# Performance work log

Measured on AMD Instinct MI355X. Metric: run time of the kernel, lower is better.

## Reference

```python
import jax, jax.numpy as jnp
import numpy as np

H, DH, RK, RD = 16, 128, 512, 64  # num_heads, head_dim, kv_lora_rank, rope_dim


def apply_rope(x, cos, sin):
    # x: [..., L, ..., rope_dim]; cos/sin: [L, rope_dim//2]
    cos = cos[None, :, None, :]
    sin = sin[None, :, None, :]
    x1, x2 = x[..., 0::2], x[..., 1::2]
    out_real = x1 * cos - x2 * sin
    out_imag = x1 * sin + x2 * cos
    return jnp.stack([out_real, out_imag], axis=-1).reshape(x.shape)


def setup_inputs() -> dict:
    key = jax.random.key(0)
    ks = jax.random.split(key, 7)
    B, L, E, MAXLEN = 2, 2048, 2048, 4096
    x = jax.random.normal(ks[0], (B, L, E), dtype=jnp.float32)
    cos_table = jax.random.uniform(ks[1], (MAXLEN, RD // 2), dtype=jnp.float32)
    sin_table = jax.random.uniform(ks[2], (MAXLEN, RD // 2), dtype=jnp.float32)
    wq = jax.random.normal(ks[3], (E, H * (DH + RD)), dtype=jnp.float32) / np.sqrt(E)
    wkv_down = jax.random.normal(ks[4], (E, RK + RD), dtype=jnp.float32) / np.sqrt(E)
    w_up = jax.random.normal(ks[5], (RK, H * (2 * DH + RD)), dtype=jnp.float32) / np.sqrt(RK)
    w_out = jax.random.normal(ks[6], (H * (DH + RD), E), dtype=jnp.float32) / np.sqrt(H * (DH + RD))
    return {"x": x, "cos_table": cos_table, "sin_table": sin_table,
            "wq": wq, "wkv_down": wkv_down, "w_up": w_up, "w_out": w_out}


def reference(x, cos_table, sin_table, wq, wkv_down, w_up, w_out):
    # Prefill path (use_cache=False): idx = 0, kv comes from current tokens only.
    B, L, E = x.shape
    cos = cos_table[:L]
    sin = sin_table[:L]

    # Queries: per-head content part + rope part
    q_all = (x @ wq).reshape(B, L, H, DH + RD)
    q_head, q_rope = q_all[..., :DH], q_all[..., DH:]
    q_rope = apply_rope(q_rope, cos, sin)
    q = jnp.concatenate([q_head, q_rope], axis=-1)  # [B,L,H,DH+RD]

    # Compressed KV latent + shared rope key
    kv_lat = x @ wkv_down                            # [B,L,RK+RD]
    c_kv = kv_lat[..., :RK]
    k_rope = kv_lat[..., RK:]
    k_rope = apply_rope(k_rope[:, :, None, :], cos, sin)[:, :, 0, :]  # [B,L,RD]

    # Up-project latent to per-head K/V
    up = (c_kv @ w_up).reshape(B, L, H, 2 * DH + RD)
    k_head = up[..., :DH]
    v_head = up[..., DH:2 * DH]
    v_rope = up[..., 2 * DH:]
    k_rope_b = jnp.broadcast_to(k_rope[:, :, None, :], (B, L, H, RD))
    k = jnp.concatenate([k_head, k_rope_b], axis=-1)  # [B,L,H,DH+RD]
    v = jnp.concatenate([v_head, v_rope], axis=-1)    # [B,L,H,DH+RD]

    # Causal attention (query_indices = arange(L), key_indices = arange(L))
    scale = 1.0 / jnp.sqrt(jnp.float32(DH + RD))
    scores = jnp.einsum('blhd,bshd->bhls', q, k) * scale
    idxs = jnp.arange(L)
    bias = jnp.where(idxs[:, None] >= idxs[None, :], 0.0, -1000000000.0)
    attn = jax.nn.softmax(scores + bias[None, None, :, :], axis=-1)
    out = jnp.einsum('bhls,bshd->blhd', attn, v)  # [B,L,H,DH+RD]
    return out.reshape(B, L, -1) @ w_out
```

## Files before the change

### kernel.cpp

```cpp
#include <hip/hip_runtime.h>
#include <stdint.h>

#define H_ 16
#define DH_ 128
#define RK_ 512
#define RD_ 64
#define B_ 2
#define L_ 2048
#define E_ 2048
#define DQ_ 192
#define NQ_ (H_*DQ_)
#define NKV_ 576
#define NKVP_ 640
#define QKVP_ 3840
#define NUP_ (H_*(2*DH_+RD_))
#define M_ (B_*L_)

typedef unsigned short u16;
typedef __bf16 bf16x8 __attribute__((ext_vector_type(8)));
typedef float floatx4 __attribute__((ext_vector_type(4)));

__device__ __forceinline__ u16 f2bf(float f) {
    union { float f; uint32_t u; } v; v.f = f;
    uint32_t u = v.u;
    u = (u + 0x7fffu + ((u >> 16) & 1u)) >> 16;
    return (u16)u;
}
__device__ __forceinline__ float bf2f(u16 b) {
    union { uint32_t u; float f; } v; v.u = ((uint32_t)b) << 16; return v.f;
}

__device__ __forceinline__ void gld_lds16(const void* g, void* l) {
    __builtin_amdgcn_global_load_lds((__attribute__((address_space(1))) void*)(g),
                                     (__attribute__((address_space(3))) void*)(l),
                                     16, 0, 0);
}

__global__ void convert_bf16(const float* __restrict__ in, u16* __restrict__ out, int n4) {
    int i = blockIdx.x * blockDim.x + threadIdx.x;
    if (i >= n4) return;
    float4 v = ((const float4*)in)[i];
    uint2 o;
    o.x = (uint32_t)f2bf(v.x) | ((uint32_t)f2bf(v.y) << 16);
    o.y = (uint32_t)f2bf(v.z) | ((uint32_t)f2bf(v.w) << 16);
    ((uint2*)out)[i] = o;
}

__global__ void transpose_w(const float* __restrict__ W, u16* __restrict__ Wt,
                            int K, int N, int Npad) {
    __shared__ float tile[32][33];
    int n0 = blockIdx.x * 32, k0 = blockIdx.y * 32;
    int tx = threadIdx.x, ty = threadIdx.y;
    for (int i = 0; i < 4; i++) {
        int k = k0 + ty + i * 8, n = n0 + tx;
        tile[ty + i * 8][tx] = (n < N) ? W[(size_t)k * N + n] : 0.f;
    }
    __syncthreads();
    for (int i = 0; i < 4; i++) {
        int n = n0 + ty + i * 8, k = k0 + tx;
        Wt[(size_t)n * K + k] = f2bf(tile[tx][ty + i * 8]);
    }
}

__global__ __launch_bounds__(256) void gemm_bt(const u16* __restrict__ A,
                                               const u16* __restrict__ Bt,
                                               float* __restrict__ C,
                                               int M, int N, int K) {
    __shared__ __align__(16) u16 As[128 * 32];
    __shared__ __align__(16) u16 Bs[128 * 32];
    const int tid = threadIdx.x;
    const int wave = tid >> 6, lane = tid & 63;
    const int quad = lane >> 4, l16 = lane & 15;
    const int m0 = blockIdx.y * 128, n0 = blockIdx.x * 128;
    const int wm = (wave >> 1) * 64, wn = (wave & 1) * 64;

    floatx4 zero4 = {0.f, 0.f, 0.f, 0.f};
    floatx4 acc[4][4];
    for (int i = 0; i < 4; i++) for (int j = 0; j < 4; j++) acc[i][j] = zero4;

    const u16* Ab = A + (size_t)m0 * K;
    const u16* Bb = Bt + (size_t)n0 * K;

    for (int k0 = 0; k0 < K; k0 += 32) {
        for (int it = 0; it < 2; ++it) {
            int c = it * 256 + tid;
            int row = c >> 2, cr = c & 3;
            gld_lds16(Ab + (size_t)row * K + k0 + cr * 8, As + c * 8);
            gld_lds16(Bb + (size_t)row * K + k0 + cr * 8, Bs + c * 8);
        }
        __syncthreads();
        bf16x8 af[4], bfr[4];
        for (int i = 0; i < 4; i++) af[i]  = *(const bf16x8*)(As + (wm + i * 16 + l16) * 32 + quad * 8);
        for (int j = 0; j < 4; j++) bfr[j] = *(const bf16x8*)(Bs + (wn + j * 16 + l16) * 32 + quad * 8);
        for (int i = 0; i < 4; i++)
            for (int j = 0; j < 4; j++)
                acc[i][j] = __builtin_amdgcn_mfma_f32_16x16x32_bf16(af[i], bfr[j], acc[i][j], 0, 0, 0);
        __syncthreads();
    }
    for (int i = 0; i < 4; i++)
        for (int j = 0; j < 4; j++) {
            int mrow = m0 + wm + i * 16 + quad * 4;
            int ncol = n0 + wn + j * 16 + l16;
            float* Cp = C + (size_t)mrow * N + ncol;
            for (int r = 0; r < 4; r++) Cp[(size_t)r * N] = acc[i][j][r];
        }
}

__global__ __launch_bounds__(512, 4) void gemm256(const u16* __restrict__ A,
                                                  const u16* __restrict__ Bt,
                                                  float* __restrict__ C,
                                                  int M, int N, int K) {
    __shared__ __align__(16) u16 As[3][256 * 32];
    __shared__ __align__(16) u16 Bs[3][128 * 32];
    const int tid = threadIdx.x;
    const int wave = tid >> 6, lane = tid & 63;
    const int quad = lane >> 4, l16 = lane & 15;
    const int wm = (wave >> 1) * 64, wn = (wave & 1) * 64;

    int nwg = gridDim.x * gridDim.y;
    int flat = blockIdx.y * gridDim.x + blockIdx.x;
    int q = nwg >> 3, r = nwg & 7;
    int xcd = flat & 7, pos = flat >> 3;
    int wg = (xcd < r) ? xcd * (q + 1) + pos : r * (q + 1) + (xcd - r) * q + pos;
    const int m0 = (wg & 15) * 256;
    const int n0 = (wg >> 4) * 128;

    const u16* Ab = A + (size_t)m0 * K;
    const u16* Bb = Bt + (size_t)n0 * K;

    const int qsw = (quad ^ ((l16 >> 1) & 3)) * 8;

    floatx4 zero4 = {0.f, 0.f, 0.f, 0.f};
    floatx4 acc[4][4];
#pragma unroll
    for (int i = 0; i < 4; i++)
#pragma unroll
        for (int j = 0; j < 4; j++) acc[i][j] = zero4;

    auto stage = [&](int t, int b) {
        const u16* Ak = Ab + t * 32;
        const u16* Bk = Bb + t * 32;
#pragma unroll
        for (int it = 0; it < 2; ++it) {
            int c = it * 512 + tid;
            int row = c >> 2, blk = c & 3;
            int bg = blk ^ ((row >> 1) & 3);
            gld_lds16(Ak + (size_t)row * K + bg * 8, As[b] + row * 32 + blk * 8);
        }
        {
            int row = tid >> 2, blk = tid & 3;
            int bg = blk ^ ((row >> 1) & 3);
            gld_lds16(Bk + (size_t)row * K + bg * 8, Bs[b] + row * 32 + blk * 8);
        }
    };

    const int NT = K >> 5;
    stage(0, 0);
    stage(1, 1);
    int rb = 0;
    for (int t = 0; t < NT; ++t) {
        if (t + 2 < NT) {
            stage(t + 2, rb ? rb - 1 : 2);
            asm volatile("s_waitcnt vmcnt(6)" ::: "memory");
        } else if (t + 1 < NT) {
            asm volatile("s_waitcnt vmcnt(3)" ::: "memory");
        } else {
            asm volatile("s_waitcnt vmcnt(0)" ::: "memory");
        }
        __builtin_amdgcn_s_barrier();

        const u16* Ar = As[rb];
        const u16* Br = Bs[rb];
        bf16x8 af[4], bfv[4];
#pragma unroll
        for (int i = 0; i < 4; i++) af[i]  = *(const bf16x8*)(Ar + (wm + i * 16 + l16) * 32 + qsw);
#pragma unroll
        for (int j = 0; j < 4; j++) bfv[j] = *(const bf16x8*)(Br + (wn + j * 16 + l16) * 32 + qsw);
        __builtin_amdgcn_s_setprio(1);
#pragma unroll
        for (int i = 0; i < 4; i++)
#pragma unroll
            for (int j = 0; j < 4; j++)
                acc[i][j] = __builtin_amdgcn_mfma_f32_16x16x32_bf16(af[i], bfv[j], acc[i][j], 0, 0, 0);
        __builtin_amdgcn_s_setprio(0);
        __builtin_amdgcn_s_barrier();
        rb = (rb == 2) ? 0 : rb + 1;
    }

#pragma unroll
    for (int i = 0; i < 4; i++)
#pragma unroll
        for (int j = 0; j < 4; j++) {
            int mrow = m0 + wm + i * 16 + quad * 4;
            int ncol = n0 + wn + j * 16 + l16;
            float* Cp = C + (size_t)mrow * N + ncol;
            for (int rr = 0; rr < 4; rr++) Cp[(size_t)rr * N] = acc[i][j][rr];
        }
}

__global__ void build_q(const float* __restrict__ qkv, const float* __restrict__ cosT,
                        const float* __restrict__ sinT, u16* __restrict__ qb) {
    const float QS = 0.07216878364870323f * 1.4426950408889634f;
    int idx = blockIdx.x * blockDim.x + threadIdx.x;
    if (idx >= M_ * H_ * 96) return;
    int p = idx % 96; int t = idx / 96; int h = t % H_; int row = t / H_;
    int l = row & (L_ - 1); int b = row >> 11;
    const float* src = qkv + (size_t)row * QKVP_ + h * DQ_;
    u16* dst = qb + ((size_t)(b * H_ + h) * L_ + l) * DQ_;
    int d = 2 * p;
    float x1 = src[d], x2 = src[d + 1];
    if (d < DH_) { dst[d] = f2bf(x1 * QS); dst[d + 1] = f2bf(x2 * QS); }
    else {
        int i = (d - DH_) >> 1;
        float c = cosT[(size_t)l * 32 + i], s = sinT[(size_t)l * 32 + i];
        dst[d]     = f2bf((x1 * c - x2 * s) * QS);
        dst[d + 1] = f2bf((x1 * s + x2 * c) * QS);
    }
}

__global__ void build_ckv(const float* __restrict__ qkv, const float* __restrict__ cosT,
                          const float* __restrict__ sinT, u16* __restrict__ ckv,
                          u16* __restrict__ kropeb) {
    int idx = blockIdx.x * blockDim.x + threadIdx.x;
    if (idx >= M_ * 288) return;
    int j = idx % 288; int row = idx / 288;
    int l = row & (L_ - 1);
    const float* src = qkv + (size_t)row * QKVP_ + NQ_;
    if (j < 256) {
        ckv[(size_t)row * RK_ + 2 * j]     = f2bf(src[2 * j]);
        ckv[(size_t)row * RK_ + 2 * j + 1] = f2bf(src[2 * j + 1]);
    } else {
        int i = j - 256;
        float x1 = src[RK_ + 2 * i], x2 = src[RK_ + 2 * i + 1];
        float c = cosT[(size_t)l * 32 + i], s = sinT[(size_t)l * 32 + i];
        kropeb[(size_t)row * RD_ + 2 * i]     = f2bf(x1 * c - x2 * s);
        kropeb[(size_t)row * RD_ + 2 * i + 1] = f2bf(x1 * s + x2 * c);
    }
}

__global__ __launch_bounds__(256) void build_kvt(const float* __restrict__ up,
        const u16* __restrict__ kropeb, u16* __restrict__ kb, u16* __restrict__ vtb) {
    __shared__ float vt[64][193];
    int blk = blockIdx.x;
    int lt = blk & 31; int bh = blk >> 5; int h = bh % H_; int b = bh / H_;
    int tid = threadIdx.x;
    int l0 = lt * 64;
    for (int it = 0; it < 48; ++it) {
        int idx = it * 256 + tid;
        int lr = idx / 192, d = idx % 192;
        size_t row = (size_t)b * L_ + l0 + lr;
        float vv = (d < DH_) ? up[row * NUP_ + h * 320 + DH_ + d]
                             : up[row * NUP_ + h * 320 + 2 * DH_ + (d - DH_)];
        vt[lr][d] = vv;
        u16 kbf = (d < DH_) ? f2bf(up[row * NUP_ + h * 320 + d])
                            : kropeb[row * RD_ + (d - DH_)];
        kb[((size_t)bh * L_ + l0 + lr) * DQ_ + d] = kbf;
    }
    __syncthreads();
    for (int it = 0; it < 48; ++it) {
        int idx = it * 256 + tid;
        int lr = idx & 63, d = idx >> 6;
        int l = l0 + lr;
        int s5 = l & 31;
        int k5 = ((s5 >> 2) & 3) * 8 + ((s5 >> 4) & 1) * 4 + (s5 & 3);
        int lp = (l & ~31) | k5;
        vtb[((size_t)bh * DQ_ + d) * L_ + lp] = f2bf(vt[lr][d]);
    }
}

__global__ __launch_bounds__(512, 2) void attn(const u16* __restrict__ qb,
        const u16* __restrict__ kb, const u16* __restrict__ vtb,
        u16* __restrict__ po0, u16* __restrict__ po1,
        float* __restrict__ pm0, float* __restrict__ pl0,
        float* __restrict__ pm1, float* __restrict__ pl1) {
    __shared__ __align__(16) u16 Ks[2][64 * 192];
    __shared__ __align__(16) u16 Vs[2][192 * 64];
    int id = blockIdx.x;
    int bh = id & 31, tj = id >> 5;
    int t = tj >> 1, j = tj & 1;
    int tid = threadIdx.x, wave = tid >> 6, lane = tid & 63;
    int quad = lane >> 4, l16 = lane & 15;

    const int x7 = l16 & 7;
    const int h2 = (x7 >> 2) & 1;
    const int qx = quad ^ (x7 & 3);
    const int oA = h2 * 32 + qx * 8;
    const int oB = (1 - h2) * 32 + qx * 8;

    u16* po = j ? po1 : po0;
    float* pm = j ? pm1 : pm0;
    float* pl = j ? pl1 : pl0;

    const u16* kbase0 = kb + (size_t)bh * L_ * DQ_;
    const u16* vbase0 = vtb + (size_t)bh * (size_t)DQ_ * L_;
    floatx4 zero4 = {0.f, 0.f, 0.f, 0.f};

    auto stageKV = [&](int st, int buf) {
        const u16* kg = kbase0 + (size_t)st * 64 * DQ_;
        u16* kd = &Ks[buf][0];
        for (int it = 0; it < 3; ++it) {
            int c = it * 512 + tid;
            int s = c / 24, blk = c - s * 24;
            int blog = (blk & 24) | ((blk & 7) ^ (s & 7));
            gld_lds16(kg + (size_t)s * DQ_ + blog * 8, kd + c * 8);
        }
        const u16* vg = vbase0 + st * 64;
        u16* vd = &Vs[buf][0];
        for (int it = 0; it < 3; ++it) {
            int c = it * 512 + tid;
            int d = c >> 3, blk = c & 7;
            int blog = blk ^ (d & 7);
            gld_lds16(vg + (size_t)d * L_ + blog * 8, vd + c * 8);
        }
    };

    for (int seg = 0; seg < 2; ++seg) {
        const int QT = seg == 0 ? (7 - t) : t;
        const int st0 = j ? (2 * QT + 2) : 0;
        const int st1 = j ? (4 * QT + 3) : (2 * QT + 1);

        bf16x8 aq[2][6];
        const u16* qbase = qb + ((size_t)bh * L_ + QT * 256 + wave * 16 + l16) * DQ_;
        for (int a = 0; a < 2; a++)
            for (int kk = 0; kk < 6; kk++)
                aq[a][kk] = *(const bf16x8*)(qbase + a * 128 * DQ_ + kk * 32 + quad * 8);

        floatx4 o[2][12];
        for (int a = 0; a < 2; a++) for (int i = 0; i < 12; i++) o[a][i] = zero4;
        float m_i[2] = {-INFINITY, -INFINITY};
        float l_i[2] = {0.f, 0.f};

        int cur = 0;
        stageKV(st0, 0);

        for (int st = st0; st <= st1; ++st) {
            if (st < st1) {
                stageKV(st + 1, cur ^ 1);
                asm volatile("s_waitcnt vmcnt(6)" ::: "memory");
            } else {
                asm volatile("s_waitcnt vmcnt(0)" ::: "memory");
            }
            __builtin_amdgcn_s_barrier();
            const u16* Kc = &Ks[cur][0];
            const u16* Vc = &Vs[cur][0];

            int R0 = QT * 256 + wave * 16 - st * 64;
            int R1 = R0 + 128;
            int smax0 = min(3, (R0 + 15) >> 4);
            int smax1 = min(3, (R1 + 15) >> 4);
            bool live0 = smax0 >= 0, live1 = smax1 >= 0;

            float pv[2][4][4];
            float mxa[2] = {-INFINITY, -INFINITY};
#pragma unroll
            for (int stile = 0; stile < 4; ++stile) {
                if (stile > smax1) {
                    for (int r = 0; r < 4; r++) { pv[0][stile][r] = 0.f; pv[1][stile][r] = 0.f; }
                    continue;
                }
                bool do0 = (stile <= smax0);
                floatx4 s1v = zero4, s0v = zero4;
#pragma unroll
                for (int kk = 0; kk < 6; kk++) {
                    int off = (kk >> 1) * 64 + ((kk & 1) ? oB : oA);
                    bf16x8 kf = *(const bf16x8*)(Kc + (stile * 16 + l16) * 192 + off);
                    s1v = __builtin_amdgcn_mfma_f32_16x16x32_bf16(kf, aq[1][kk], s1v, 0, 0, 0);
                    if (do0) s0v = __builtin_amdgcn_mfma_f32_16x16x32_bf16(kf, aq[0][kk], s0v, 0, 0, 0);
                }
                int sb = stile * 16;
                if (sb + 15 > R1) {
                    for (int r = 0; r < 4; r++) {
                        float v = (sb + quad * 4 + r > R1 + l16) ? -1e30f : s1v[r];
                        pv[1][stile][r] = v; mxa[1] = fmaxf(mxa[1], v);
                    }
                } else {
                    for (int r = 0; r < 4; r++) { pv[1][stile][r] = s1v[r]; mxa[1] = fmaxf(mxa[1], s1v[r]); }
                }
                if (do0) {
                    if (sb + 15 > R0) {
                        for (int r = 0; r < 4; r++) {
                            float v = (sb + quad * 4 + r > R0 + l16) ? -1e30f : s0v[r];
                            pv[0][stile][r] = v; mxa[0] = fmaxf(mxa[0], v);
                        }
                    } else {
                        for (int r = 0; r < 4; r++) { pv[0][stile][r] = s0v[r]; mxa[0] = fmaxf(mxa[0], s0v[r]); }
                    }
                } else {
                    for (int r = 0; r < 4; r++) pv[0][stile][r] = 0.f;
                }
            }

            bf16x8 pf[2][2];
            bool lv[2] = {live0, live1};
            int smx[2] = {smax0, smax1};
#pragma unroll
            for (int a = 0; a < 2; a++) {
                if (!lv[a]) continue;
                float mx = mxa[a];
                mx = fmaxf(mx, __shfl_xor(mx, 16));
                mx = fmaxf(mx, __shfl_xor(mx, 32));
                float mn;
                if (__all(mx <= m_i[a] + 8.0f)) {
                    mn = m_i[a];
                } else {
                    mn = fmaxf(m_i[a], mx);
                    float alpha = exp2f(m_i[a] - mn);
                    m_i[a] = mn;
                    l_i[a] *= alpha;
                    for (int i = 0; i < 12; i++) o[a][i] *= alpha;
                }
                float rs = 0.f;
#pragma unroll
                for (int stile = 0; stile < 4; ++stile) {
                    if (stile > smx[a]) continue;
                    for (int r = 0; r < 4; r++) {
                        float e = exp2f(pv[a][stile][r] - mn);
                        pv[a][stile][r] = e;
                        rs += e;
                    }
                }
                rs += __shfl_xor(rs, 16);
                rs += __shfl_xor(rs, 32);
                l_i[a] += rs;
                for (int g = 0; g < 2; g++) {
                    union { bf16x8 v; u16 s[8]; } u;
                    for (int r = 0; r < 4; r++) {
                        u.s[r]     = f2bf(pv[a][g * 2][r]);
                        u.s[4 + r] = f2bf(pv[a][g * 2 + 1][r]);
                    }
                    pf[a][g] = u.v;
                }
            }

            for (int g = 0; g < 2; g++) {
                int vo = g ? oB : oA;
#pragma unroll
                for (int dtile = 0; dtile < 12; dtile++) {
                    bf16x8 vf = *(const bf16x8*)(Vc + (dtile * 16 + l16) * 64 + vo);
                    if (live0)
                        o[0][dtile] = __builtin_amdgcn_mfma_f32_16x16x32_bf16(vf, pf[0][g], o[0][dtile], 0, 0, 0);
                    if (live1)
                        o[1][dtile] = __builtin_amdgcn_mfma_f32_16x16x32_bf16(vf, pf[1][g], o[1][dtile], 0, 0, 0);
                }
            }
            __builtin_amdgcn_s_barrier();
            cur ^= 1;
        }

        int tile = bh * 8 + QT;
        for (int a = 0; a < 2; a++) {
            int q = a * 128 + wave * 16 + l16;
            u16* dst = po + ((size_t)tile * 256 + q) * 192;
            for (int dtile = 0; dtile < 12; dtile++) {
                ushort4 pk;
                pk.x = f2bf(o[a][dtile][0]);
                pk.y = f2bf(o[a][dtile][1]);
                pk.z = f2bf(o[a][dtile][2]);
                pk.w = f2bf(o[a][dtile][3]);
                *(ushort4*)(dst + dtile * 16 + quad * 4) = pk;
            }
            if (quad == 0) {
                pm[(size_t)tile * 256 + q] = m_i[a];
                pl[(size_t)tile * 256 + q] = l_i[a];
            }
        }
        __syncthreads();
    }
}

__global__ void attn_merge(const u16* __restrict__ po0, const u16* __restrict__ po1,
                           const float* __restrict__ pm0, const float* __restrict__ pl0,
                           const float* __restrict__ pm1, const float* __restrict__ pl1,
                           u16* __restrict__ ao) {
    int idx = blockIdx.x * blockDim.x + threadIdx.x;
    int c = idx % 48; int rest = idx / 48;
    int q = rest & 255; int tile = rest >> 8;
    int bh = tile >> 3, QT = tile & 7;
    size_t mi = (size_t)tile * 256 + q;
    float m0 = pm0[mi], m1 = pm1[mi];
    float l0 = pl0[mi], l1 = pl1[mi];
    float m = fmaxf(m0, m1);
    float a0 = exp2f(m0 - m), a1 = exp2f(m1 - m);
    float inv = 1.0f / (l0 * a0 + l1 * a1);
    float s0 = a0 * inv, s1 = a1 * inv;
    ushort4 u0 = *(const ushort4*)(po0 + mi * 192 + c * 4);
    ushort4 u1 = *(const ushort4*)(po1 + mi * 192 + c * 4);
    int b = bh >> 4, h = bh & 15;
    int l = QT * 256 + q;
    u16* dst = ao + (((size_t)(b * L_ + l)) * H_ + h) * DQ_ + c * 4;
    ushort4 pk;
    pk.x = f2bf(bf2f(u0.x) * s0 + bf2f(u1.x) * s1);
    pk.y = f2bf(bf2f(u0.y) * s0 + bf2f(u1.y) * s1);
    pk.z = f2bf(bf2f(u0.z) * s0 + bf2f(u1.z) * s1);
    pk.w = f2bf(bf2f(u0.w) * s0 + bf2f(u1.w) * s1);
    *(ushort4*)dst = pk;
}

extern "C" void kernel_launch(void* const* d_in, const int* in_sizes, int n_in,
                              void* d_out, int out_size, void* d_ws, size_t ws_size,
                              hipStream_t stream) {
    const float* x    = (const float*)d_in[0];
    const float* cosT = (const float*)d_in[1];
    const float* sinT = (const float*)d_in[2];
    const float* wq   = (const float*)d_in[3];
    const float* wkv  = (const float*)d_in[4];
    const float* wup  = (const float*)d_in[5];
    const float* wout = (const float*)d_in[6];
    float* out = (float*)d_out;
    char* ws = (char*)d_ws;

    size_t off = 0;
    auto alloc = [&](size_t b) { size_t r = off; off += (b + 255) & ~(size_t)255; return r; };
    u16* xb     = (u16*)(ws + alloc((size_t)M_ * E_ * 2));
    u16* wqkvT  = (u16*)(ws + alloc((size_t)QKVP_ * E_ * 2));
    u16* wupT   = (u16*)(ws + alloc((size_t)NUP_ * RK_ * 2));
    u16* woutT  = (u16*)(ws + alloc((size_t)E_ * NQ_ * 2));
    u16* qb     = (u16*)(ws + alloc((size_t)B_ * H_ * L_ * DQ_ * 2));
    u16* kb     = (u16*)(ws + alloc((size_t)B_ * H_ * L_ * DQ_ * 2));
    u16* vtb    = (u16*)(ws + alloc((size_t)B_ * H_ * DQ_ * L_ * 2));
    u16* ao     = (u16*)(ws + alloc((size_t)M_ * NQ_ * 2));
    u16* ckv    = (u16*)(ws + alloc((size_t)M_ * RK_ * 2));
    u16* kropeb = (u16*)(ws + alloc((size_t)M_ * RD_ * 2));
    char* scratch = ws + alloc((size_t)M_ * NUP_ * 4);
    float* qkv = (float*)(scratch);
    float* up  = (float*)(scratch);
    size_t poSz = (size_t)256 * 256 * 192 * 2;
    u16*   po0 = (u16*)(scratch);
    u16*   po1 = (u16*)(scratch + poSz);
    float* pm0 = (float*)(scratch + 2 * poSz);
    float* pl0 = (float*)(scratch + 2 * poSz + 256 * 256 * 4);
    float* pm1 = (float*)(scratch + 2 * poSz + 2 * 256 * 256 * 4);
    float* pl1 = (float*)(scratch + 2 * poSz + 3 * 256 * 256 * 4);

    dim3 tb(32, 8);
    int n4 = M_ * E_ / 4;
    convert_bf16<<<(n4 + 255) / 256, 256, 0, stream>>>(x, xb, n4);
    transpose_w<<<dim3(NQ_ / 32, E_ / 32), tb, 0, stream>>>(wq, wqkvT, E_, NQ_, NQ_);
    transpose_w<<<dim3((QKVP_ - NQ_) / 32, E_ / 32), tb, 0, stream>>>(wkv, wqkvT + (size_t)NQ_ * E_, E_, NKV_, QKVP_ - NQ_);
    transpose_w<<<dim3(NUP_ / 32, RK_ / 32), tb, 0, stream>>>(wup, wupT, RK_, NUP_, NUP_);
    transpose_w<<<dim3(E_ / 32, NQ_ / 32), tb, 0, stream>>>(wout, woutT, NQ_, E_, E_);

    gemm256<<<dim3(QKVP_ / 128, M_ / 256), 512, 0, stream>>>(xb, wqkvT, qkv, M_, QKVP_, E_);

    int nq = M_ * H_ * 96;
    build_q<<<(nq + 255) / 256, 256, 0, stream>>>(qkv, cosT, sinT, qb);
    int nc = M_ * 288;
    build_ckv<<<(nc + 255) / 256, 256, 0, stream>>>(qkv, cosT, sinT, ckv, kropeb);

    gemm_bt<<<dim3(NUP_ / 128, M_ / 128), 256, 0, stream>>>(ckv, wupT, up, M_, NUP_, RK_);
    build_kvt<<<B_ * H_ * 32, 256, 0, stream>>>(up, kropeb, kb, vtb);

    attn<<<256, 512, 0, stream>>>(qb, kb, vtb, po0, po1, pm0, pl0, pm1, pl1);
    attn_merge<<<(256 * 256 * 48) / 256, 256, 0, stream>>>(po0, po1, pm0, pl0, pm1, pl1, ao);

    gemm256<<<dim3(E_ / 128, M_ / 256), 512, 0, stream>>>(ao, woutT, out, M_, E_, NQ_);
}
```

Before: 584.8 us.

## Merge launches, use packed bf16 conversion, reuse gemm256 for up-projection, interleave softmax with PV

The four weight-transpose launches become one combined kernel, and build_q and build_ckv become one kernel, which cuts launch count. The simple gemm_bt for the up-projection is replaced by the pipelined gemm256. Manual bf16 rounding is replaced by the hardware v_cvt_pk_bf16_f32 instruction in several kernels. In attention, the exp and pack steps are interleaved per PV group and the max reductions are restructured, which may change register pressure and scheduling.

```diff
diff --git a/kernel.cpp b/kernel.cpp
--- a/kernel.cpp
+++ b/kernel.cpp
@@ -29,6 +29,11 @@
 __device__ __forceinline__ float bf2f(u16 b) {
     union { uint32_t u; float f; } v; v.u = ((uint32_t)b) << 16; return v.f;
 }
+__device__ __forceinline__ uint32_t cvtpk(float lo, float hi) {
+    uint32_t r;
+    asm("v_cvt_pk_bf16_f32 %0, %1, %2" : "=v"(r) : "v"(lo), "v"(hi));
+    return r;
+}
 
 __device__ __forceinline__ void gld_lds16(const void* g, void* l) {
     __builtin_amdgcn_global_load_lds((__attribute__((address_space(1))) void*)(g),
@@ -41,15 +46,23 @@
     if (i >= n4) return;
     float4 v = ((const float4*)in)[i];
     uint2 o;
-    o.x = (uint32_t)f2bf(v.x) | ((uint32_t)f2bf(v.y) << 16);
-    o.y = (uint32_t)f2bf(v.z) | ((uint32_t)f2bf(v.w) << 16);
+    o.x = cvtpk(v.x, v.y);
+    o.y = cvtpk(v.z, v.w);
     ((uint2*)out)[i] = o;
 }
 
-__global__ void transpose_w(const float* __restrict__ W, u16* __restrict__ Wt,
-                            int K, int N, int Npad) {
+__global__ void transpose_all(const float* __restrict__ wq, const float* __restrict__ wkv,
+                              const float* __restrict__ wup, const float* __restrict__ wout,
+                              u16* __restrict__ wqkvT, u16* __restrict__ wupT,
+                              u16* __restrict__ woutT) {
     __shared__ float tile[32][33];
-    int n0 = blockIdx.x * 32, k0 = blockIdx.y * 32;
+    int bid = blockIdx.x;
+    const float* W; u16* Wt; int K, N, bx, by;
+    if (bid < 6144)        { W = wq;   Wt = wqkvT;                      K = 2048; N = 3072; bx = bid % 96;  by = bid / 96; }
+    else if (bid < 7680)   { int b = bid - 6144; W = wkv;  Wt = wqkvT + (size_t)3072 * 2048; K = 2048; N = 576;  bx = b % 24;  by = b / 24; }
+    else if (bid < 10240)  { int b = bid - 7680; W = wup;  Wt = wupT;   K = 512;  N = 5120; bx = b % 160; by = b / 160; }
+    else                   { int b = bid - 10240; W = wout; Wt = woutT; K = 3072; N = 2048; bx = b % 64;  by = b / 64; }
+    int n0 = bx * 32, k0 = by * 32;
     int tx = threadIdx.x, ty = threadIdx.y;
     for (int i = 0; i < 4; i++) {
         int k = k0 + ty + i * 8, n = n0 + tx;
@@ -60,50 +73,6 @@
         int n = n0 + ty + i * 8, k = k0 + tx;
         Wt[(size_t)n * K + k] = f2bf(tile[tx][ty + i * 8]);
     }
-}
-
-__global__ __launch_bounds__(256) void gemm_bt(const u16* __restrict__ A,
-                                               const u16* __restrict__ Bt,
-                                               float* __restrict__ C,
-                                               int M, int N, int K) {
-    __shared__ __align__(16) u16 As[128 * 32];
-    __shared__ __align__(16) u16 Bs[128 * 32];
-    const int tid = threadIdx.x;
-    const int wave = tid >> 6, lane = tid & 63;
-    const int quad = lane >> 4, l16 = lane & 15;
-    const int m0 = blockIdx.y * 128, n0 = blockIdx.x * 128;
-    const int wm = (wave >> 1) * 64, wn = (wave & 1) * 64;
-
-    floatx4 zero4 = {0.f, 0.f, 0.f, 0.f};
-    floatx4 acc[4][4];
-    for (int i = 0; i < 4; i++) for (int j = 0; j < 4; j++) acc[i][j] = zero4;
-
-    const u16* Ab = A + (size_t)m0 * K;
-    const u16* Bb = Bt + (size_t)n0 * K;
-
-    for (int k0 = 0; k0 < K; k0 += 32) {
-        for (int it = 0; it < 2; ++it) {
-            int c = it * 256 + tid;
-            int row = c >> 2, cr = c & 3;
-            gld_lds16(Ab + (size_t)row * K + k0 + cr * 8, As + c * 8);
-            gld_lds16(Bb + (size_t)row * K + k0 + cr * 8, Bs + c * 8);
-        }
-        __syncthreads();
-        bf16x8 af[4], bfr[4];
-        for (int i = 0; i < 4; i++) af[i]  = *(const bf16x8*)(As + (wm + i * 16 + l16) * 32 + quad * 8);
-        for (int j = 0; j < 4; j++) bfr[j] = *(const bf16x8*)(Bs + (wn + j * 16 + l16) * 32 + quad * 8);
-        for (int i = 0; i < 4; i++)
-            for (int j = 0; j < 4; j++)
-                acc[i][j] = __builtin_amdgcn_mfma_f32_16x16x32_bf16(af[i], bfr[j], acc[i][j], 0, 0, 0);
-        __syncthreads();
-    }
-    for (int i = 0; i < 4; i++)
-        for (int j = 0; j < 4; j++) {
-            int mrow = m0 + wm + i * 16 + quad * 4;
-            int ncol = n0 + wn + j * 16 + l16;
-            float* Cp = C + (size_t)mrow * N + ncol;
-            for (int r = 0; r < 4; r++) Cp[(size_t)r * N] = acc[i][j][r];
-        }
 }
 
 __global__ __launch_bounds__(512, 4) void gemm256(const u16* __restrict__ A,
@@ -198,43 +167,42 @@
         }
 }
 
-__global__ void build_q(const float* __restrict__ qkv, const float* __restrict__ cosT,
-                        const float* __restrict__ sinT, u16* __restrict__ qb) {
+__global__ void build_qckv(const float* __restrict__ qkv, const float* __restrict__ cosT,
+                           const float* __restrict__ sinT, u16* __restrict__ qb,
+                           u16* __restrict__ ckv, u16* __restrict__ kropeb) {
     const float QS = 0.07216878364870323f * 1.4426950408889634f;
     int idx = blockIdx.x * blockDim.x + threadIdx.x;
-    if (idx >= M_ * H_ * 96) return;
-    int p = idx % 96; int t = idx / 96; int h = t % H_; int row = t / H_;
-    int l = row & (L_ - 1); int b = row >> 11;
-    const float* src = qkv + (size_t)row * QKVP_ + h * DQ_;
-    u16* dst = qb + ((size_t)(b * H_ + h) * L_ + l) * DQ_;
-    int d = 2 * p;
-    float x1 = src[d], x2 = src[d + 1];
-    if (d < DH_) { dst[d] = f2bf(x1 * QS); dst[d + 1] = f2bf(x2 * QS); }
-    else {
-        int i = (d - DH_) >> 1;
-        float c = cosT[(size_t)l * 32 + i], s = sinT[(size_t)l * 32 + i];
-        dst[d]     = f2bf((x1 * c - x2 * s) * QS);
-        dst[d + 1] = f2bf((x1 * s + x2 * c) * QS);
-    }
-}
-
-__global__ void build_ckv(const float* __restrict__ qkv, const float* __restrict__ cosT,
-                          const float* __restrict__ sinT, u16* __restrict__ ckv,
-                          u16* __restrict__ kropeb) {
-    int idx = blockIdx.x * blockDim.x + threadIdx.x;
-    if (idx >= M_ * 288) return;
-    int j = idx % 288; int row = idx / 288;
-    int l = row & (L_ - 1);
-    const float* src = qkv + (size_t)row * QKVP_ + NQ_;
-    if (j < 256) {
-        ckv[(size_t)row * RK_ + 2 * j]     = f2bf(src[2 * j]);
-        ckv[(size_t)row * RK_ + 2 * j + 1] = f2bf(src[2 * j + 1]);
+    const int NQTH = M_ * H_ * 96;
+    if (idx < NQTH) {
+        int p = idx % 96; int t = idx / 96; int h = t % H_; int row = t / H_;
+        int l = row & (L_ - 1); int b = row >> 11;
+        const float* src = qkv + (size_t)row * QKVP_ + h * DQ_;
+        u16* dst = qb + ((size_t)(b * H_ + h) * L_ + l) * DQ_;
+        int d = 2 * p;
+        float x1 = src[d], x2 = src[d + 1];
+        if (d < DH_) { dst[d] = f2bf(x1 * QS); dst[d + 1] = f2bf(x2 * QS); }
+        else {
+            int i = (d - DH_) >> 1;
+            float c = cosT[(size_t)l * 32 + i], s = sinT[(size_t)l * 32 + i];
+            dst[d]     = f2bf((x1 * c - x2 * s) * QS);
+            dst[d + 1] = f2bf((x1 * s + x2 * c) * QS);
+        }
     } else {
-        int i = j - 256;
-        float x1 = src[RK_ + 2 * i], x2 = src[RK_ + 2 * i + 1];
-        float c = cosT[(size_t)l * 32 + i], s = sinT[(size_t)l * 32 + i];
-        kropeb[(size_t)row * RD_ + 2 * i]     = f2bf(x1 * c - x2 * s);
-        kropeb[(size_t)row * RD_ + 2 * i + 1] = f2bf(x1 * s + x2 * c);
+        idx -= NQTH;
+        if (idx >= M_ * 288) return;
+        int j = idx % 288; int row = idx / 288;
+        int l = row & (L_ - 1);
+        const float* src = qkv + (size_t)row * QKVP_ + NQ_;
+        if (j < 256) {
+            ckv[(size_t)row * RK_ + 2 * j]     = f2bf(src[2 * j]);
+            ckv[(size_t)row * RK_ + 2 * j + 1] = f2bf(src[2 * j + 1]);
+        } else {
+            int i = j - 256;
+            float x1 = src[RK_ + 2 * i], x2 = src[RK_ + 2 * i + 1];
+            float c = cosT[(size_t)l * 32 + i], s = sinT[(size_t)l * 32 + i];
+            kropeb[(size_t)row * RD_ + 2 * i]     = f2bf(x1 * c - x2 * s);
+            kropeb[(size_t)row * RD_ + 2 * i + 1] = f2bf(x1 * s + x2 * c);
+        }
     }
 }
 
@@ -369,33 +337,41 @@
                 }
                 int sb = stile * 16;
                 if (sb + 15 > R1) {
-                    for (int r = 0; r < 4; r++) {
-                        float v = (sb + quad * 4 + r > R1 + l16) ? -1e30f : s1v[r];
-                        pv[1][stile][r] = v; mxa[1] = fmaxf(mxa[1], v);
-                    }
+                    float v0 = (sb + quad * 4 + 0 > R1 + l16) ? -1e30f : s1v[0];
+                    float v1 = (sb + quad * 4 + 1 > R1 + l16) ? -1e30f : s1v[1];
+                    float v2 = (sb + quad * 4 + 2 > R1 + l16) ? -1e30f : s1v[2];
+                    float v3 = (sb + quad * 4 + 3 > R1 + l16) ? -1e30f : s1v[3];
+                    pv[1][stile][0] = v0; pv[1][stile][1] = v1;
+                    pv[1][stile][2] = v2; pv[1][stile][3] = v3;
+                    mxa[1] = fmaxf(mxa[1], fmaxf(fmaxf(v0, v1), fmaxf(v2, v3)));
                 } else {
-                    for (int r = 0; r < 4; r++) { pv[1][stile][r] = s1v[r]; mxa[1] = fmaxf(mxa[1], s1v[r]); }
+                    for (int r = 0; r < 4; r++) pv[1][stile][r] = s1v[r];
+                    mxa[1] = fmaxf(mxa[1], fmaxf(fmaxf(s1v[0], s1v[1]), fmaxf(s1v[2], s1v[3])));
                 }
                 if (do0) {
                     if (sb + 15 > R0) {
-                        for (int r = 0; r < 4; r++) {
-                            float v = (sb + quad * 4 + r > R0 + l16) ? -1e30f : s0v[r];
-                            pv[0][stile][r] = v; mxa[0] = fmaxf(mxa[0], v);
-                        }
+                        float v0 = (sb + quad * 4 + 0 > R0 + l16) ? -1e30f : s0v[0];
+                        float v1 = (sb + quad * 4 + 1 > R0 + l16) ? -1e30f : s0v[1];
+                        float v2 = (sb + quad * 4 + 2 > R0 + l16) ? -1e30f : s0v[2];
+                        float v3 = (sb + quad * 4 + 3 > R0 + l16) ? -1e30f : s0v[3];
+                        pv[0][stile][0] = v0; pv[0][stile][1] = v1;
+                        pv[0][stile][2] = v2; pv[0][stile][3] = v3;
+                        mxa[0] = fmaxf(mxa[0], fmaxf(fmaxf(v0, v1), fmaxf(v2, v3)));
                     } else {
-                        for (int r = 0; r < 4; r++) { pv[0][stile][r] = s0v[r]; mxa[0] = fmaxf(mxa[0], s0v[r]); }
+                        for (int r = 0; r < 4; r++) pv[0][stile][r] = s0v[r];
+                        mxa[0] = fmaxf(mxa[0], fmaxf(fmaxf(s0v[0], s0v[1]), fmaxf(s0v[2], s0v[3])));
                     }
                 } else {
                     for (int r = 0; r < 4; r++) pv[0][stile][r] = 0.f;
                 }
             }
 
-            bf16x8 pf[2][2];
-            bool lv[2] = {live0, live1};
-            int smx[2] = {smax0, smax1};
+            bool lvA[2] = {live0, live1};
+            int smxA[2] = {smax0, smax1};
+            float mn_[2];
 #pragma unroll
             for (int a = 0; a < 2; a++) {
-                if (!lv[a]) continue;
+                if (!lvA[a]) { mn_[a] = 0.f; continue; }
                 float mx = mxa[a];
                 mx = fmaxf(mx, __shfl_xor(mx, 16));
                 mx = fmaxf(mx, __shfl_xor(mx, 32));
@@ -409,39 +385,55 @@
                     l_i[a] *= alpha;
                     for (int i = 0; i < 12; i++) o[a][i] *= alpha;
                 }
-                float rs = 0.f;
-#pragma unroll
-                for (int stile = 0; stile < 4; ++stile) {
-                    if (stile > smx[a]) continue;
-                    for (int r = 0; r < 4; r++) {
-                        float e = exp2f(pv[a][stile][r] - mn);
-                        pv[a][stile][r] = e;
-                        rs += e;
+                mn_[a] = mn;
+            }
+
+            float rs[2] = {0.f, 0.f};
+#pragma unroll
+            for (int g = 0; g < 2; g++) {
+                bf16x8 pfg[2];
+#pragma unroll
+                for (int a = 0; a < 2; a++) {
+                    uint32_t d0 = 0, d1 = 0, d2 = 0, d3 = 0;
+                    if (lvA[a]) {
+                        if (2 * g <= smxA[a]) {
+                            float e0 = exp2f(pv[a][2 * g][0] - mn_[a]);
+                            float e1 = exp2f(pv[a][2 * g][1] - mn_[a]);
+                            float e2 = exp2f(pv[a][2 * g][2] - mn_[a]);
+                            float e3 = exp2f(pv[a][2 * g][3] - mn_[a]);
+                            rs[a] += (e0 + e1) + (e2 + e3);
+                            d0 = cvtpk(e0, e1); d1 = cvtpk(e2, e3);
+                        }
+                        if (2 * g + 1 <= smxA[a]) {
+                            float e4 = exp2f(pv[a][2 * g + 1][0] - mn_[a]);
+                            float e5 = exp2f(pv[a][2 * g + 1][1] - mn_[a]);
+                            float e6 = exp2f(pv[a][2 * g + 1][2] - mn_[a]);
+                            float e7 = exp2f(pv[a][2 * g + 1][3] - mn_[a]);
+                            rs[a] += (e4 + e5) + (e6 + e7);
+                            d2 = cvtpk(e4, e5); d3 = cvtpk(e6, e7);
+                        }
                     }
-                }
-                rs += __shfl_xor(rs, 16);
-                rs += __shfl_xor(rs, 32);
-                l_i[a] += rs;
-                for (int g = 0; g < 2; g++) {
-                    union { bf16x8 v; u16 s[8]; } u;
-                    for (int r = 0; r < 4; r++) {
-                        u.s[r]     = f2bf(pv[a][g * 2][r]);
-                        u.s[4 + r] = f2bf(pv[a][g * 2 + 1][r]);
-                    }
-                    pf[a][g] = u.v;
-                }
-            }
-
-            for (int g = 0; g < 2; g++) {
+                    union { bf16x8 v; uint32_t d[4]; } u;
+                    u.d[0] = d0; u.d[1] = d1; u.d[2] = d2; u.d[3] = d3;
+                    pfg[a] = u.v;
+                }
                 int vo = g ? oB : oA;
 #pragma unroll
                 for (int dtile = 0; dtile < 12; dtile++) {
                     bf16x8 vf = *(const bf16x8*)(Vc + (dtile * 16 + l16) * 64 + vo);
                     if (live0)
-                        o[0][dtile] = __builtin_amdgcn_mfma_f32_16x16x32_bf16(vf, pf[0][g], o[0][dtile], 0, 0, 0);
+                        o[0][dtile] = __builtin_amdgcn_mfma_f32_16x16x32_bf16(vf, pfg[0], o[0][dtile], 0, 0, 0);
                     if (live1)
-                        o[1][dtile] = __builtin_amdgcn_mfma_f32_16x16x32_bf16(vf, pf[1][g], o[1][dtile], 0, 0, 0);
-                }
+                        o[1][dtile] = __builtin_amdgcn_mfma_f32_16x16x32_bf16(vf, pfg[1], o[1][dtile], 0, 0, 0);
+                }
+            }
+#pragma unroll
+            for (int a = 0; a < 2; a++) {
+                if (!lvA[a]) continue;
+                float r2 = rs[a];
+                r2 += __shfl_xor(r2, 16);
+                r2 += __shfl_xor(r2, 32);
+                l_i[a] += r2;
             }
             __builtin_amdgcn_s_barrier();
             cur ^= 1;
@@ -452,12 +444,10 @@
             int q = a * 128 + wave * 16 + l16;
             u16* dst = po + ((size_t)tile * 256 + q) * 192;
             for (int dtile = 0; dtile < 12; dtile++) {
-                ushort4 pk;
-                pk.x = f2bf(o[a][dtile][0]);
-                pk.y = f2bf(o[a][dtile][1]);
-                pk.z = f2bf(o[a][dtile][2]);
-                pk.w = f2bf(o[a][dtile][3]);
-                *(ushort4*)(dst + dtile * 16 + quad * 4) = pk;
+                uint2 pk2;
+                pk2.x = cvtpk(o[a][dtile][0], o[a][dtile][1]);
+                pk2.y = cvtpk(o[a][dtile][2], o[a][dtile][3]);
+                *(uint2*)(dst + dtile * 16 + quad * 4) = pk2;
             }
             if (quad == 0) {
                 pm[(size_t)tile * 256 + q] = m_i[a];
@@ -488,12 +478,10 @@
     int b = bh >> 4, h = bh & 15;
     int l = QT * 256 + q;
     u16* dst = ao + (((size_t)(b * L_ + l)) * H_ + h) * DQ_ + c * 4;
-    ushort4 pk;
-    pk.x = f2bf(bf2f(u0.x) * s0 + bf2f(u1.x) * s1);
-    pk.y = f2bf(bf2f(u0.y) * s0 + bf2f(u1.y) * s1);
-    pk.z = f2bf(bf2f(u0.z) * s0 + bf2f(u1.z) * s1);
-    pk.w = f2bf(bf2f(u0.w) * s0 + bf2f(u1.w) * s1);
-    *(ushort4*)dst = pk;
+    uint2 pk2;
+    pk2.x = cvtpk(bf2f(u0.x) * s0 + bf2f(u1.x) * s1, bf2f(u0.y) * s0 + bf2f(u1.y) * s1);
+    pk2.y = cvtpk(bf2f(u0.z) * s0 + bf2f(u1.z) * s1, bf2f(u0.w) * s0 + bf2f(u1.w) * s1);
+    *(uint2*)dst = pk2;
 }
 
 extern "C" void kernel_launch(void* const* d_in, const int* in_sizes, int n_in,
@@ -535,19 +523,14 @@
     dim3 tb(32, 8);
     int n4 = M_ * E_ / 4;
     convert_bf16<<<(n4 + 255) / 256, 256, 0, stream>>>(x, xb, n4);
-    transpose_w<<<dim3(NQ_ / 32, E_ / 32), tb, 0, stream>>>(wq, wqkvT, E_, NQ_, NQ_);
-    transpose_w<<<dim3((QKVP_ - NQ_) / 32, E_ / 32), tb, 0, stream>>>(wkv, wqkvT + (size_t)NQ_ * E_, E_, NKV_, QKVP_ - NQ_);
-    transpose_w<<<dim3(NUP_ / 32, RK_ / 32), tb, 0, stream>>>(wup, wupT, RK_, NUP_, NUP_);
-    transpose_w<<<dim3(E_ / 32, NQ_ / 32), tb, 0, stream>>>(wout, woutT, NQ_, E_, E_);
+    transpose_all<<<16384, tb, 0, stream>>>(wq, wkv, wup, wout, wqkvT, wupT, woutT);
 
     gemm256<<<dim3(QKVP_ / 128, M_ / 256), 512, 0, stream>>>(xb, wqkvT, qkv, M_, QKVP_, E_);
 
-    int nq = M_ * H_ * 96;
-    build_q<<<(nq + 255) / 256, 256, 0, stream>>>(qkv, cosT, sinT, qb);
-    int nc = M_ * 288;
-    build_ckv<<<(nc + 255) / 256, 256, 0, stream>>>(qkv, cosT, sinT, ckv, kropeb);
-
-    gemm_bt<<<dim3(NUP_ / 128, M_ / 128), 256, 0, stream>>>(ckv, wupT, up, M_, NUP_, RK_);
+    int nb = (M_ * H_ * 96 + M_ * 288) / 256;
+    build_qckv<<<nb, 256, 0, stream>>>(qkv, cosT, sinT, qb, ckv, kropeb);
+
+    gemm256<<<dim3(NUP_ / 128, M_ / 256), 512, 0, stream>>>(ckv, wupT, up, M_, NUP_, RK_);
     build_kvt<<<B_ * H_ * 32, 256, 0, stream>>>(up, kropeb, kb, vtb);
 
     attn<<<256, 512, 0, stream>>>(qb, kb, vtb, po0, po1, pm0, pl0, pm1, pl1);
```

Result: faster. 549.3 us (-6.1%).

## Emit bf16 from projection GEMMs, fuse prep kernels, reuse gemm256 for up-projection

Applied to the files above, without the earlier changes.

Projection GEMMs now write bf16 instead of fp32, which halves intermediate traffic for qkv and up. The up-projection reads the latent slice of qkv directly through a leading-dimension parameter, so the separate ckv conversion buffer and the simple gemm_bt kernel are dropped. The q and k_rope builders are merged into one kernel, the four weight transposes run as a single launch, and packed hardware bf16 conversion is used in several places. This adds rounding of intermediates to bf16 earlier, and the up GEMM now uses the larger 256-row tile kernel.

```diff
diff --git a/kernel.cpp b/kernel.cpp
--- a/kernel.cpp
+++ b/kernel.cpp
@@ -11,7 +11,6 @@
 #define DQ_ 192
 #define NQ_ (H_*DQ_)
 #define NKV_ 576
-#define NKVP_ 640
 #define QKVP_ 3840
 #define NUP_ (H_*(2*DH_+RD_))
 #define M_ (B_*L_)
@@ -29,6 +28,11 @@
 __device__ __forceinline__ float bf2f(u16 b) {
     union { uint32_t u; float f; } v; v.u = ((uint32_t)b) << 16; return v.f;
 }
+__device__ __forceinline__ uint32_t cvtpk(float lo, float hi) {
+    uint32_t r;
+    asm("v_cvt_pk_bf16_f32 %0, %1, %2" : "=v"(r) : "v"(lo), "v"(hi));
+    return r;
+}
 
 __device__ __forceinline__ void gld_lds16(const void* g, void* l) {
     __builtin_amdgcn_global_load_lds((__attribute__((address_space(1))) void*)(g),
@@ -41,15 +45,23 @@
     if (i >= n4) return;
     float4 v = ((const float4*)in)[i];
     uint2 o;
-    o.x = (uint32_t)f2bf(v.x) | ((uint32_t)f2bf(v.y) << 16);
-    o.y = (uint32_t)f2bf(v.z) | ((uint32_t)f2bf(v.w) << 16);
+    o.x = cvtpk(v.x, v.y);
+    o.y = cvtpk(v.z, v.w);
     ((uint2*)out)[i] = o;
 }
 
-__global__ void transpose_w(const float* __restrict__ W, u16* __restrict__ Wt,
-                            int K, int N, int Npad) {
+__global__ void transpose_all(const float* __restrict__ wq, const float* __restrict__ wkv,
+                              const float* __restrict__ wup, const float* __restrict__ wout,
+                              u16* __restrict__ wqkvT, u16* __restrict__ wupT,
+                              u16* __restrict__ woutT) {
     __shared__ float tile[32][33];
-    int n0 = blockIdx.x * 32, k0 = blockIdx.y * 32;
+    int bid = blockIdx.x;
+    const float* W; u16* Wt; int K, N, bx, by;
+    if (bid < 6144)        { W = wq;   Wt = wqkvT;                      K = 2048; N = 3072; bx = bid % 96;  by = bid / 96; }
+    else if (bid < 7680)   { int b = bid - 6144; W = wkv;  Wt = wqkvT + (size_t)3072 * 2048; K = 2048; N = 576;  bx = b % 24;  by = b / 24; }
+    else if (bid < 10240)  { int b = bid - 7680; W = wup;  Wt = wupT;   K = 512;  N = 5120; bx = b % 160; by = b / 160; }
+    else                   { int b = bid - 10240; W = wout; Wt = woutT; K = 3072; N = 2048; bx = b % 64;  by = b / 64; }
+    int n0 = bx * 32, k0 = by * 32;
     int tx = threadIdx.x, ty = threadIdx.y;
     for (int i = 0; i < 4; i++) {
         int k = k0 + ty + i * 8, n = n0 + tx;
@@ -62,54 +74,11 @@
     }
 }
 
-__global__ __launch_bounds__(256) void gemm_bt(const u16* __restrict__ A,
-                                               const u16* __restrict__ Bt,
-                                               float* __restrict__ C,
-                                               int M, int N, int K) {
-    __shared__ __align__(16) u16 As[128 * 32];
-    __shared__ __align__(16) u16 Bs[128 * 32];
-    const int tid = threadIdx.x;
-    const int wave = tid >> 6, lane = tid & 63;
-    const int quad = lane >> 4, l16 = lane & 15;
-    const int m0 = blockIdx.y * 128, n0 = blockIdx.x * 128;
-    const int wm = (wave >> 1) * 64, wn = (wave & 1) * 64;
-
-    floatx4 zero4 = {0.f, 0.f, 0.f, 0.f};
-    floatx4 acc[4][4];
-    for (int i = 0; i < 4; i++) for (int j = 0; j < 4; j++) acc[i][j] = zero4;
-
-    const u16* Ab = A + (size_t)m0 * K;
-    const u16* Bb = Bt + (size_t)n0 * K;
-
-    for (int k0 = 0; k0 < K; k0 += 32) {
-        for (int it = 0; it < 2; ++it) {
-            int c = it * 256 + tid;
-            int row = c >> 2, cr = c & 3;
-            gld_lds16(Ab + (size_t)row * K + k0 + cr * 8, As + c * 8);
-            gld_lds16(Bb + (size_t)row * K + k0 + cr * 8, Bs + c * 8);
-        }
-        __syncthreads();
-        bf16x8 af[4], bfr[4];
-        for (int i = 0; i < 4; i++) af[i]  = *(const bf16x8*)(As + (wm + i * 16 + l16) * 32 + quad * 8);
-        for (int j = 0; j < 4; j++) bfr[j] = *(const bf16x8*)(Bs + (wn + j * 16 + l16) * 32 + quad * 8);
-        for (int i = 0; i < 4; i++)
-            for (int j = 0; j < 4; j++)
-                acc[i][j] = __builtin_amdgcn_mfma_f32_16x16x32_bf16(af[i], bfr[j], acc[i][j], 0, 0, 0);
-        __syncthreads();
-    }
-    for (int i = 0; i < 4; i++)
-        for (int j = 0; j < 4; j++) {
-            int mrow = m0 + wm + i * 16 + quad * 4;
-            int ncol = n0 + wn + j * 16 + l16;
-            float* Cp = C + (size_t)mrow * N + ncol;
-            for (int r = 0; r < 4; r++) Cp[(size_t)r * N] = acc[i][j][r];
-        }
-}
-
+template<bool BF16OUT>
 __global__ __launch_bounds__(512, 4) void gemm256(const u16* __restrict__ A,
                                                   const u16* __restrict__ Bt,
-                                                  float* __restrict__ C,
-                                                  int M, int N, int K) {
+                                                  void* __restrict__ Cv,
+                                                  int M, int N, int K, int lda) {
     __shared__ __align__(16) u16 As[3][256 * 32];
     __shared__ __align__(16) u16 Bs[3][128 * 32];
     const int tid = threadIdx.x;
@@ -125,7 +94,7 @@
     const int m0 = (wg & 15) * 256;
     const int n0 = (wg >> 4) * 128;
 
-    const u16* Ab = A + (size_t)m0 * K;
+    const u16* Ab = A + (size_t)m0 * lda;
     const u16* Bb = Bt + (size_t)n0 * K;
 
     const int qsw = (quad ^ ((l16 >> 1) & 3)) * 8;
@@ -145,7 +114,7 @@
             int c = it * 512 + tid;
             int row = c >> 2, blk = c & 3;
             int bg = blk ^ ((row >> 1) & 3);
-            gld_lds16(Ak + (size_t)row * K + bg * 8, As[b] + row * 32 + blk * 8);
+            gld_lds16(Ak + (size_t)row * lda + bg * 8, As[b] + row * 32 + blk * 8);
         }
         {
             int row = tid >> 2, blk = tid & 3;
@@ -193,54 +162,53 @@
         for (int j = 0; j < 4; j++) {
             int mrow = m0 + wm + i * 16 + quad * 4;
             int ncol = n0 + wn + j * 16 + l16;
-            float* Cp = C + (size_t)mrow * N + ncol;
-            for (int rr = 0; rr < 4; rr++) Cp[(size_t)rr * N] = acc[i][j][rr];
-        }
-}
-
-__global__ void build_q(const float* __restrict__ qkv, const float* __restrict__ cosT,
-                        const float* __restrict__ sinT, u16* __restrict__ qb) {
+            if (BF16OUT) {
+                u16* Cp = (u16*)Cv + (size_t)mrow * N + ncol;
+                for (int rr = 0; rr < 4; rr++) Cp[(size_t)rr * N] = f2bf(acc[i][j][rr]);
+            } else {
+                float* Cp = (float*)Cv + (size_t)mrow * N + ncol;
+                for (int rr = 0; rr < 4; rr++) Cp[(size_t)rr * N] = acc[i][j][rr];
+            }
+        }
+}
+
+__global__ void build_qckv(const u16* __restrict__ qkv, const float* __restrict__ cosT,
+                           const float* __restrict__ sinT, u16* __restrict__ qb,
+                           u16* __restrict__ kropeb) {
     const float QS = 0.07216878364870323f * 1.4426950408889634f;
     int idx = blockIdx.x * blockDim.x + threadIdx.x;
-    if (idx >= M_ * H_ * 96) return;
-    int p = idx % 96; int t = idx / 96; int h = t % H_; int row = t / H_;
-    int l = row & (L_ - 1); int b = row >> 11;
-    const float* src = qkv + (size_t)row * QKVP_ + h * DQ_;
-    u16* dst = qb + ((size_t)(b * H_ + h) * L_ + l) * DQ_;
-    int d = 2 * p;
-    float x1 = src[d], x2 = src[d + 1];
-    if (d < DH_) { dst[d] = f2bf(x1 * QS); dst[d + 1] = f2bf(x2 * QS); }
-    else {
-        int i = (d - DH_) >> 1;
+    const int NQTH = M_ * H_ * 96;
+    if (idx < NQTH) {
+        int p = idx % 96; int t = idx / 96; int h = t % H_; int row = t / H_;
+        int l = row & (L_ - 1); int b = row >> 11;
+        const u16* src = qkv + (size_t)row * QKVP_ + h * DQ_;
+        u16* dst = qb + ((size_t)(b * H_ + h) * L_ + l) * DQ_;
+        int d = 2 * p;
+        uint32_t w = *(const uint32_t*)(src + d);
+        float x1 = bf2f((u16)(w & 0xffff)), x2 = bf2f((u16)(w >> 16));
+        uint32_t o;
+        if (d < DH_) o = cvtpk(x1 * QS, x2 * QS);
+        else {
+            int i = (d - DH_) >> 1;
+            float c = cosT[(size_t)l * 32 + i], s = sinT[(size_t)l * 32 + i];
+            o = cvtpk((x1 * c - x2 * s) * QS, (x1 * s + x2 * c) * QS);
+        }
+        *(uint32_t*)(dst + d) = o;
+    } else {
+        idx -= NQTH;
+        if (idx >= M_ * 32) return;
+        int i = idx & 31; int row = idx >> 5;
+        int l = row & (L_ - 1);
+        uint32_t w = *(const uint32_t*)(qkv + (size_t)row * QKVP_ + NQ_ + RK_ + 2 * i);
+        float x1 = bf2f((u16)(w & 0xffff)), x2 = bf2f((u16)(w >> 16));
         float c = cosT[(size_t)l * 32 + i], s = sinT[(size_t)l * 32 + i];
-        dst[d]     = f2bf((x1 * c - x2 * s) * QS);
-        dst[d + 1] = f2bf((x1 * s + x2 * c) * QS);
-    }
-}
-
-__global__ void build_ckv(const float* __restrict__ qkv, const float* __restrict__ cosT,
-                          const float* __restrict__ sinT, u16* __restrict__ ckv,
-                          u16* __restrict__ kropeb) {
-    int idx = blockIdx.x * blockDim.x + threadIdx.x;
-    if (idx >= M_ * 288) return;
-    int j = idx % 288; int row = idx / 288;
-    int l = row & (L_ - 1);
-    const float* src = qkv + (size_t)row * QKVP_ + NQ_;
-    if (j < 256) {
-        ckv[(size_t)row * RK_ + 2 * j]     = f2bf(src[2 * j]);
-        ckv[(size_t)row * RK_ + 2 * j + 1] = f2bf(src[2 * j + 1]);
-    } else {
-        int i = j - 256;
-        float x1 = src[RK_ + 2 * i], x2 = src[RK_ + 2 * i + 1];
-        float c = cosT[(size_t)l * 32 + i], s = sinT[(size_t)l * 32 + i];
-        kropeb[(size_t)row * RD_ + 2 * i]     = f2bf(x1 * c - x2 * s);
-        kropeb[(size_t)row * RD_ + 2 * i + 1] = f2bf(x1 * s + x2 * c);
-    }
-}
-
-__global__ __launch_bounds__(256) void build_kvt(const float* __restrict__ up,
+        *(uint32_t*)(kropeb + (size_t)row * RD_ + 2 * i) = cvtpk(x1 * c - x2 * s, x1 * s + x2 * c);
+    }
+}
+
+__global__ __launch_bounds__(256) void build_kvt(const u16* __restrict__ up,
         const u16* __restrict__ kropeb, u16* __restrict__ kb, u16* __restrict__ vtb) {
-    __shared__ float vt[64][193];
+    __shared__ u16 vt[64][193];
     int blk = blockIdx.x;
     int lt = blk & 31; int bh = blk >> 5; int h = bh % H_; int b = bh / H_;
     int tid = threadIdx.x;
@@ -249,10 +217,10 @@
         int idx = it * 256 + tid;
         int lr = idx / 192, d = idx % 192;
         size_t row = (size_t)b * L_ + l0 + lr;
-        float vv = (d < DH_) ? up[row * NUP_ + h * 320 + DH_ + d]
-                             : up[row * NUP_ + h * 320 + 2 * DH_ + (d - DH_)];
+        u16 vv = (d < DH_) ? up[row * NUP_ + h * 320 + DH_ + d]
+                           : up[row * NUP_ + h * 320 + 2 * DH_ + (d - DH_)];
         vt[lr][d] = vv;
-        u16 kbf = (d < DH_) ? f2bf(up[row * NUP_ + h * 320 + d])
+        u16 kbf = (d < DH_) ? up[row * NUP_ + h * 320 + d]
                             : kropeb[row * RD_ + (d - DH_)];
         kb[((size_t)bh * L_ + l0 + lr) * DQ_ + d] = kbf;
     }
@@ -264,7 +232,7 @@
         int s5 = l & 31;
         int k5 = ((s5 >> 2) & 3) * 8 + ((s5 >> 4) & 1) * 4 + (s5 & 3);
         int lp = (l & ~31) | k5;
-        vtb[((size_t)bh * DQ_ + d) * L_ + lp] = f2bf(vt[lr][d]);
+        vtb[((size_t)bh * DQ_ + d) * L_ + lp] = vt[lr][d];
     }
 }
 
@@ -488,12 +456,10 @@
     int b = bh >> 4, h = bh & 15;
     int l = QT * 256 + q;
     u16* dst = ao + (((size_t)(b * L_ + l)) * H_ + h) * DQ_ + c * 4;
-    ushort4 pk;
-    pk.x = f2bf(bf2f(u0.x) * s0 + bf2f(u1.x) * s1);
-    pk.y = f2bf(bf2f(u0.y) * s0 + bf2f(u1.y) * s1);
-    pk.z = f2bf(bf2f(u0.z) * s0 + bf2f(u1.z) * s1);
-    pk.w = f2bf(bf2f(u0.w) * s0 + bf2f(u1.w) * s1);
-    *(ushort4*)dst = pk;
+    uint2 pk2;
+    pk2.x = cvtpk(bf2f(u0.x) * s0 + bf2f(u1.x) * s1, bf2f(u0.y) * s0 + bf2f(u1.y) * s1);
+    pk2.y = cvtpk(bf2f(u0.z) * s0 + bf2f(u1.z) * s1, bf2f(u0.w) * s0 + bf2f(u1.w) * s1);
+    *(uint2*)dst = pk2;
 }
 
 extern "C" void kernel_launch(void* const* d_in, const int* in_sizes, int n_in,
@@ -519,11 +485,11 @@
     u16* kb     = (u16*)(ws + alloc((size_t)B_ * H_ * L_ * DQ_ * 2));
     u16* vtb    = (u16*)(ws + alloc((size_t)B_ * H_ * DQ_ * L_ * 2));
     u16* ao     = (u16*)(ws + alloc((size_t)M_ * NQ_ * 2));
-    u16* ckv    = (u16*)(ws + alloc((size_t)M_ * RK_ * 2));
     u16* kropeb = (u16*)(ws + alloc((size_t)M_ * RD_ * 2));
     char* scratch = ws + alloc((size_t)M_ * NUP_ * 4);
-    float* qkv = (float*)(scratch);
-    float* up  = (float*)(scratch);
+    u16* qkvb = (u16*)(scratch);
+    size_t qkvSz = ((size_t)M_ * QKVP_ * 2 + 255) & ~(size_t)255;
+    u16* upb  = (u16*)(scratch + qkvSz);
     size_t poSz = (size_t)256 * 256 * 192 * 2;
     u16*   po0 = (u16*)(scratch);
     u16*   po1 = (u16*)(scratch + poSz);
@@ -535,23 +501,18 @@
     dim3 tb(32, 8);
     int n4 = M_ * E_ / 4;
     convert_bf16<<<(n4 + 255) / 256, 256, 0, stream>>>(x, xb, n4);
-    transpose_w<<<dim3(NQ_ / 32, E_ / 32), tb, 0, stream>>>(wq, wqkvT, E_, NQ_, NQ_);
-    transpose_w<<<dim3((QKVP_ - NQ_) / 32, E_ / 32), tb, 0, stream>>>(wkv, wqkvT + (size_t)NQ_ * E_, E_, NKV_, QKVP_ - NQ_);
-    transpose_w<<<dim3(NUP_ / 32, RK_ / 32), tb, 0, stream>>>(wup, wupT, RK_, NUP_, NUP_);
-    transpose_w<<<dim3(E_ / 32, NQ_ / 32), tb, 0, stream>>>(wout, woutT, NQ_, E_, E_);
-
-    gemm256<<<dim3(QKVP_ / 128, M_ / 256), 512, 0, stream>>>(xb, wqkvT, qkv, M_, QKVP_, E_);
-
-    int nq = M_ * H_ * 96;
-    build_q<<<(nq + 255) / 256, 256, 0, stream>>>(qkv, cosT, sinT, qb);
-    int nc = M_ * 288;
-    build_ckv<<<(nc + 255) / 256, 256, 0, stream>>>(qkv, cosT, sinT, ckv, kropeb);
-
-    gemm_bt<<<dim3(NUP_ / 128, M_ / 128), 256, 0, stream>>>(ckv, wupT, up, M_, NUP_, RK_);
-    build_kvt<<<B_ * H_ * 32, 256, 0, stream>>>(up, kropeb, kb, vtb);
+    transpose_all<<<16384, tb, 0, stream>>>(wq, wkv, wup, wout, wqkvT, wupT, woutT);
+
+    gemm256<true><<<dim3(QKVP_ / 128, M_ / 256), 512, 0, stream>>>(xb, wqkvT, qkvb, M_, QKVP_, E_, E_);
+
+    int nb = (M_ * H_ * 96 + M_ * 32 + 255) / 256;
+    build_qckv<<<nb, 256, 0, stream>>>(qkvb, cosT, sinT, qb, kropeb);
+
+    gemm256<true><<<dim3(NUP_ / 128, M_ / 256), 512, 0, stream>>>(qkvb + NQ_, wupT, upb, M_, NUP_, RK_, QKVP_);
+    build_kvt<<<B_ * H_ * 32, 256, 0, stream>>>(upb, kropeb, kb, vtb);
 
     attn<<<256, 512, 0, stream>>>(qb, kb, vtb, po0, po1, pm0, pl0, pm1, pl1);
     attn_merge<<<(256 * 256 * 48) / 256, 256, 0, stream>>>(po0, po1, pm0, pl0, pm1, pl1, ao);
 
-    gemm256<<<dim3(E_ / 128, M_ / 256), 512, 0, stream>>>(ao, woutT, out, M_, E_, NQ_);
-}
+    gemm256<false><<<dim3(E_ / 128, M_ / 256), 512, 0, stream>>>(ao, woutT, out, M_, E_, NQ_, NQ_);
+}
```

Result: faster. 494.4 us (-15.5%).
